# Performance work log

Hardware: AMD Instinct MI355X
Metric: run time of the kernel (lower is better)

Reference implementation:

```python
import jax, jax.numpy as jnp
import numpy as np

NUM_HEADS = 8


def setup_inputs() -> dict:
    key = jax.random.key(0)
    ks = jax.random.split(key, 8)
    B, N, D, H = 4, 1200, 256, NUM_HEADS
    return {
        "query_bbox": jax.random.normal(ks[0], (B, N, 10), jnp.float32) * 20.0,
        "query_feat": jax.random.normal(ks[1], (B, N, D), jnp.float32),
        "beta_w": jax.random.normal(ks[2], (H, D), jnp.float32) * 0.02,
        "beta_b": jax.random.uniform(ks[3], (H,), jnp.float32, 0.0, 2.0),
        "in_proj_w": jax.random.normal(ks[4], (3 * D, D), jnp.float32) * (D ** -0.5),
        "in_proj_b": jnp.zeros((3 * D,), jnp.float32),
        "out_proj_w": jax.random.normal(ks[5], (D, D), jnp.float32) * (D ** -0.5),
        "out_proj_b": jnp.zeros((D,), jnp.float32),
    }


def reference(query_bbox, query_feat, beta_w, beta_b, in_proj_w, in_proj_b,
              out_proj_w, out_proj_b):
    B, N, D = query_feat.shape
    H = NUM_HEADS
    hd = D // H

    # center_dists (no_grad in original): negative pairwise L2 of bbox centers
    centers = jax.lax.stop_gradient(query_bbox[..., :2])            # [B,N,2]
    diff = centers[:, :, None, :] - centers[:, None, :, :]          # [B,N,N,2]
    dist = -jnp.sqrt(jnp.sum(diff * diff, axis=-1))                 # [B,N,N]

    # per-head learned beta scale
    beta = jnp.einsum('bnd,hd->bhn', query_feat, beta_w) + beta_b[None, :, None]  # [B,H,N]
    attn_mask = dist[:, None, :, :] * beta[..., None]               # [B,H,N,N]

    # multi-head self-attention with additive mask
    qkv = jnp.einsum('bnd,ed->bne', query_feat, in_proj_w) + in_proj_b
    q, k, v = jnp.split(qkv, 3, axis=-1)
    q = q.reshape(B, N, H, hd)
    k = k.reshape(B, N, H, hd)
    v = v.reshape(B, N, H, hd)

    scores = jnp.einsum('bqhd,bkhd->bhqk', q, k) * (hd ** -0.5) + attn_mask
    attn = jax.nn.softmax(scores, axis=-1)                          # [B,H,N,N]
    out = jnp.einsum('bhqk,bkhd->bqhd', attn, v).reshape(B, N, D)
    return jnp.einsum('bnd,ed->bne', out, out_proj_w) + out_proj_b
```

## Files before the change

### kernel.cpp

```cpp
#include <hip/hip_runtime.h>
#include <hip/hip_bf16.h>

#define BC 4
#define NQ 1200
#define DIM 256
#define NH 8
#define HD 32
#define E3 768
#define MROWS (BC*NQ)
#define SCALE 0.17677669529663687f
#define L2E 1.4426950408889634f
#define SL2E (SCALE * L2E)

#define VT2_PER_BH 40960
#define VT2_PER_HH 20480

typedef __attribute__((ext_vector_type(8))) short bf16x8;
typedef __attribute__((ext_vector_type(4))) float f32x4;
typedef __attribute__((ext_vector_type(2))) unsigned u32x2;
typedef __attribute__((ext_vector_type(4))) unsigned u32x4;

__device__ inline short f2bf(float f) {
    __hip_bfloat16 h = __float2bfloat16(f);
    return *reinterpret_cast<short*>(&h);
}
__device__ __forceinline__ unsigned cvtpk(float lo, float hi) {
    unsigned r;
    asm("v_cvt_pk_bf16_f32 %0, %1, %2" : "=v"(r) : "v"(lo), "v"(hi));
    return r;
}

__device__ __forceinline__ void gll16(const void* g, void* l) {
    __builtin_amdgcn_global_load_lds(
        (const __attribute__((address_space(1))) unsigned*)g,
        (__attribute__((address_space(3))) unsigned*)l, 16, 0, 0);
}

__global__ void beta_ctr_kernel(const float* __restrict__ feat, const float* __restrict__ bw,
                                const float* __restrict__ bb, const float* __restrict__ bbox,
                                float* __restrict__ beta, float* __restrict__ ctr) {
    int gw = (blockIdx.x * 256 + threadIdx.x) >> 6;
    int lane = threadIdx.x & 63;
    if (gw >= MROWS) return;
    const float* frow = feat + (size_t)gw * DIM;
    float acc[NH];
#pragma unroll
    for (int h = 0; h < NH; ++h) acc[h] = 0.f;
#pragma unroll
    for (int it = 0; it < DIM / 64; ++it) {
        int d = it * 64 + lane;
        float f = frow[d];
#pragma unroll
        for (int h = 0; h < NH; ++h) acc[h] += f * bw[h * DIM + d];
    }
#pragma unroll
    for (int h = 0; h < NH; ++h) {
#pragma unroll
        for (int off = 32; off; off >>= 1) acc[h] += __shfl_xor(acc[h], off);
    }
    int b = gw / NQ, n = gw % NQ;
#pragma unroll
    for (int h = 0; h < NH; ++h) {
        float v = acc[h] + bb[h];
        if (lane == h) beta[(b * NH + h) * NQ + n] = v;
    }
    if (lane == 0) {
        ctr[gw * 2]     = bbox[(size_t)gw * 10];
        ctr[gw * 2 + 1] = bbox[(size_t)gw * 10 + 1];
    }
}

template<bool AF32, bool BF32, bool OUTF32, bool VTOUT, bool QSCALE>
__global__ __launch_bounds__(256) void gemm_k256(const void* __restrict__ Av,
                                                 const void* __restrict__ Bv,
                                                 const float* __restrict__ bias,
                                                 void* __restrict__ Cout, int Edim,
                                                 short* __restrict__ vtout) {
    __shared__ short as[64][40];
    __shared__ short bs[64][40];
    int m0 = blockIdx.y * 64, e0 = blockIdx.x * 64;
    int t = threadIdx.x, lane = t & 63, wid = t >> 6;
    int wr = (wid >> 1) * 32, wc = (wid & 1) * 32;
    f32x4 acc[2][2] = {};
    int lrow = t >> 2, lch = t & 3;
    const float qs = (QSCALE && e0 < DIM) ? SL2E : 1.f;

    for (int ks = 0; ks < DIM / 32; ++ks) {
        bf16x8 av, wv;
        if (AF32) {
            const float* A = (const float*)Av;
            float4 f0 = *(const float4*)(A + (size_t)(m0 + lrow) * DIM + ks * 32 + lch * 8);
            float4 f1 = *(const float4*)(A + (size_t)(m0 + lrow) * DIM + ks * 32 + lch * 8 + 4);
            u32x4 p = {cvtpk(f0.x, f0.y), cvtpk(f0.z, f0.w),
                       cvtpk(f1.x, f1.y), cvtpk(f1.z, f1.w)};
            av = __builtin_bit_cast(bf16x8, p);
        } else {
            av = *(const bf16x8*)((const short*)Av + (size_t)(m0 + lrow) * DIM + ks * 32 + lch * 8);
        }
        if (BF32) {
            const float* B = (const float*)Bv;
            float4 f0 = *(const float4*)(B + (size_t)(e0 + lrow) * DIM + ks * 32 + lch * 8);
            float4 f1 = *(const float4*)(B + (size_t)(e0 + lrow) * DIM + ks * 32 + lch * 8 + 4);
            u32x4 p = {cvtpk(f0.x * qs, f0.y * qs), cvtpk(f0.z * qs, f0.w * qs),
                       cvtpk(f1.x * qs, f1.y * qs), cvtpk(f1.z * qs, f1.w * qs)};
            wv = __builtin_bit_cast(bf16x8, p);
        } else {
            wv = *(const bf16x8*)((const short*)Bv + (size_t)(e0 + lrow) * DIM + ks * 32 + lch * 8);
        }
        __syncthreads();
        *(bf16x8*)&as[lrow][lch * 8] = av;
        *(bf16x8*)&bs[lrow][lch * 8] = wv;
        __syncthreads();
#pragma unroll
        for (int sm = 0; sm < 2; ++sm) {
            bf16x8 af = *(const bf16x8*)&as[wr + sm * 16 + (lane & 15)][(lane >> 4) * 8];
#pragma unroll
            for (int sn = 0; sn < 2; ++sn) {
                bf16x8 bfv = *(const bf16x8*)&bs[wc + sn * 16 + (lane & 15)][(lane >> 4) * 8];
                acc[sm][sn] = __builtin_amdgcn_mfma_f32_16x16x32_bf16(af, bfv, acc[sm][sn], 0, 0, 0);
            }
        }
    }
#pragma unroll
    for (int sm = 0; sm < 2; ++sm)
#pragma unroll
        for (int sn = 0; sn < 2; ++sn) {
            int e = e0 + wc + sn * 16 + (lane & 15);
            float bv = bias[e];
            if (QSCALE && e < DIM) bv *= SL2E;
            float vals[4];
            int mbase = m0 + wr + sm * 16 + (lane >> 4) * 4;
#pragma unroll
            for (int r = 0; r < 4; ++r) vals[r] = acc[sm][sn][r] + bv;
            if (VTOUT && e >= 2 * DIM) {
                int dv = e - 2 * DIM;
                int hv = dv >> 5, dd = dv & 31;
                int hh = dd >> 4, di = dd & 15;
                int bb = mbase / NQ, nn = mbase - bb * NQ;
                u32x2 o = {cvtpk(vals[0], vals[1]), cvtpk(vals[2], vals[3])};
                size_t off = (size_t)(bb * NH + hv) * VT2_PER_BH + hh * VT2_PER_HH
                           + (nn >> 3) * 128 + di * 8 + (nn & 7);
                *(u32x2*)&vtout[off] = o;
            } else {
#pragma unroll
                for (int r = 0; r < 4; ++r) {
                    int m = mbase + r;
                    if (OUTF32) ((float*)Cout)[(size_t)m * Edim + e] = vals[r];
                    else        ((short*)Cout)[(size_t)m * Edim + e] = f2bf(vals[r]);
                }
            }
        }
}

#define BUFSZ 17408
#define KT_OFF 0
#define VT_OFF 8192
#define CK_OFF 16384
#define PL_OFF (2*BUFSZ)
__global__ __launch_bounds__(256, 4) void attn_kernel(const short* __restrict__ qkv,
                                                      const short* __restrict__ vt2,
                                                      const float* __restrict__ beta,
                                                      const float* __restrict__ ctr,
                                                      short* __restrict__ attnb) {
    __shared__ __align__(16) char smem[2 * BUFSZ + 4096];

    const int t = threadIdx.x, lane = t & 63, w = t >> 6;
    const int g = lane >> 4, i = lane & 15;
    const int qg = w >> 1, ksp = w & 1;
    const int bh = blockIdx.y, b = bh >> 3, h = bh & 7;
    const int q0 = blockIdx.x * 32 + qg * 16;
    const int q = q0 + i, qc = min(q, NQ - 1);
    const int kwb = ksp * 64;
    const int bq = b * NQ;

    bf16x8 qf = *(const bf16x8*)(qkv + (size_t)(bq + qc) * E3 + h * HD + g * 8);
    const float cqx = ctr[(bq + qc) * 2];
    const float cqy = ctr[(bq + qc) * 2 + 1];
    const float nbql = -beta[(b * NH + h) * NQ + qc] * L2E;

    const short onebf = (short)0x3F80;
    const bf16x8 ones = {onebf, onebf, onebf, onebf, onebf, onebf, onebf, onebf};

    float mcur = 0.f;
    f32x4 o0 = {}, o1 = {}, oS = {};

    const int koff = ((t >> 6) << 4) + (t & 15);
    const short* kld0 = qkv + (size_t)bq * E3 + DIM + h * HD + (size_t)koff * E3 + ((t >> 4) & 3) * 8;
    const short* kld1 = kld0 + (size_t)64 * E3;
    const short* vld0 = vt2 + (size_t)bh * VT2_PER_BH + (((t >> 4) & 15)) * 128 + (t & 15) * 8;
    const short* vld1 = vld0 + VT2_PER_HH;
    const char*  cld  = (const char*)(ctr + (size_t)bq * 2) + lane * 16;

    auto stage_issue = [&](int base) {
        gll16(kld0, &smem[base + KT_OFF + t * 16]);
        gll16(kld1, &smem[base + KT_OFF + (t + 256) * 16]);
        gll16(vld0, &smem[base + VT_OFF + t * 16]);
        gll16(vld1, &smem[base + VT_OFF + (t + 256) * 16]);
        if (w == 0) gll16(cld, &smem[base + CK_OFF + lane * 16]);
        kld0 += (size_t)128 * E3; kld1 += (size_t)128 * E3;
        vld0 += 2048; vld1 += 2048; cld += 1024;
    };

    stage_issue(0);
    __syncthreads();
    int cur = 0;

    for (int kb = 0; kb < NQ; kb += 128) {
        const bool haveNext = (kb + 128 < NQ);
        const bool tail = (kb + 128 > NQ);
        if (haveNext) stage_issue((cur ^ 1) * BUFSZ);

        const int cb = cur * BUFSZ;
        float st[16];
        f32x4 cinit = {-mcur, -mcur, -mcur, -mcur};
#pragma unroll
        for (int kcl = 0; kcl < 4; ++kcl) {
            bf16x8 af = *(const bf16x8*)&smem[cb + KT_OFF + (((ksp * 4 + kcl) * 64 + lane) << 4)];
            f32x4 s = __builtin_amdgcn_mfma_f32_16x16x32_bf16(af, qf, cinit, 0, 0, 0);
            int lk = kwb + kcl * 16 + 4 * g;
            float4 cA = *(const float4*)&smem[cb + CK_OFF + lk * 8];
            float4 cB = *(const float4*)&smem[cb + CK_OFF + lk * 8 + 16];
            float cxv[4] = {cA.x, cA.z, cB.x, cB.z};
            float cyv[4] = {cA.y, cA.w, cB.y, cB.w};
#pragma unroll
            for (int r = 0; r < 4; ++r) {
                float dx = cqx - cxv[r], dy = cqy - cyv[r];
                float d2 = __builtin_fmaf(dx, dx, dy * dy);
                float dist = __builtin_amdgcn_sqrtf(d2);
                st[kcl * 4 + r] = __builtin_fmaf(dist, nbql, s[r]);
            }
            if (tail) {
#pragma unroll
                for (int r = 0; r < 4; ++r)
                    if (kb + lk + r >= NQ) st[kcl * 4 + r] = -1e30f;
            }
        }

        float a0 = fmaxf(fmaxf(st[0],  st[1]),  st[2]);
        float a1 = fmaxf(fmaxf(st[3],  st[4]),  st[5]);
        float a2 = fmaxf(fmaxf(st[6],  st[7]),  st[8]);
        float a3 = fmaxf(fmaxf(st[9],  st[10]), st[11]);
        float a4 = fmaxf(fmaxf(st[12], st[13]), st[14]);
        float vm = fmaxf(fmaxf(fmaxf(a0, a1), a2), fmaxf(fmaxf(a3, a4), st[15]));
        if (!__all(vm <= 8.0f)) {
            float vr = fmaxf(vm, __shfl_xor(vm, 16));
            vr = fmaxf(vr, __shfl_xor(vr, 32));
            float dm = fmaxf(vr, 0.f);
            float al = __builtin_amdgcn_exp2f(-dm);
            mcur += dm;
#pragma unroll
            for (int r = 0; r < 4; ++r) { o0[r] *= al; o1[r] *= al; }
            oS[0] *= al;
#pragma unroll
            for (int x = 0; x < 16; ++x) st[x] -= dm;
        }
#pragma unroll
        for (int x = 0; x < 16; ++x) st[x] = __builtin_amdgcn_exp2f(st[x]);

#pragma unroll
        for (int kc2 = 0; kc2 < 2; ++kc2) {
#pragma unroll
            for (int kk = 0; kk < 2; ++kk) {
                int kcl = 2 * kc2 + kk;
                u32x2 pw = {cvtpk(st[kcl * 4 + 0], st[kcl * 4 + 1]),
                            cvtpk(st[kcl * 4 + 2], st[kcl * 4 + 3])};
                *(u32x2*)&smem[PL_OFF + (w << 10) + (((kk << 1) + (g >> 1)) << 8) + (i << 4) + ((g & 1) << 3)] = pw;
            }
            bf16x8 pbf = *(const bf16x8*)&smem[PL_OFF + (w << 10) + (g << 8) + (i << 4)];
            int vidx = (8 * ksp + 4 * kc2 + g) * 16 + i;
            bf16x8 vf0 = *(const bf16x8*)&smem[cb + VT_OFF + (vidx << 4)];
            bf16x8 vf1 = *(const bf16x8*)&smem[cb + VT_OFF + ((256 + vidx) << 4)];
            __builtin_amdgcn_s_setprio(1);
            o0 = __builtin_amdgcn_mfma_f32_16x16x32_bf16(vf0, pbf, o0, 0, 0, 0);
            o1 = __builtin_amdgcn_mfma_f32_16x16x32_bf16(vf1, pbf, o1, 0, 0, 0);
            oS = __builtin_amdgcn_mfma_f32_16x16x32_bf16(ones, pbf, oS, 0, 0, 0);
            __builtin_amdgcn_s_setprio(0);
        }

        __syncthreads();
        cur ^= 1;
    }

    float lsum = oS[0];
    float* mrg = (float*)smem;
    float* my = mrg + (w * 64 + lane) * 10;
    my[0] = mcur; my[1] = lsum;
#pragma unroll
    for (int r = 0; r < 4; ++r) { my[2 + r] = o0[r]; my[6 + r] = o1[r]; }
    __syncthreads();
    const float* pr = mrg + ((w ^ 1) * 64 + lane) * 10;
    float m2 = pr[0], l2 = pr[1];
    float mN = fmaxf(mcur, m2);
    float a1 = __builtin_amdgcn_exp2f(mcur - mN);
    float a2 = __builtin_amdgcn_exp2f(m2 - mN);
    float inv = 1.f / (lsum * a1 + l2 * a2);
    int hh = w & 1;
    f32x4 mine = hh ? o1 : o0;
    if (q < NQ) {
        float vals[4];
#pragma unroll
        for (int r = 0; r < 4; ++r) vals[r] = (mine[r] * a1 + pr[2 + hh * 4 + r] * a2) * inv;
        u32x2 outv = {cvtpk(vals[0], vals[1]), cvtpk(vals[2], vals[3])};
        *(u32x2*)&attnb[(size_t)(bq + q) * DIM + h * HD + hh * 16 + 4 * g] = outv;
    }
}

extern "C" void kernel_launch(void* const* d_in, const int* in_sizes, int n_in,
                              void* d_out, int out_size, void* d_ws, size_t ws_size,
                              hipStream_t stream) {
    const float* bbox  = (const float*)d_in[0];
    const float* feat  = (const float*)d_in[1];
    const float* bw    = (const float*)d_in[2];
    const float* bb    = (const float*)d_in[3];
    const float* in_w  = (const float*)d_in[4];
    const float* in_b  = (const float*)d_in[5];
    const float* out_w = (const float*)d_in[6];
    const float* out_b = (const float*)d_in[7];
    float* out = (float*)d_out;

    char* ws = (char*)d_ws;
    size_t off = 0;
    auto alloc = [&](size_t bytes) { void* p = ws + off; off += (bytes + 255) & ~255ull; return p; };
    short* qkvb  = (short*)alloc((size_t)MROWS * E3 * 2);
    short* vtb   = (short*)alloc((size_t)BC * NH * VT2_PER_BH * 2);
    short* attnb = (short*)alloc((size_t)MROWS * DIM * 2);
    float* betab = (float*)alloc((size_t)BC * NH * NQ * 4);
    float* ctr   = (float*)alloc((size_t)BC * NQ * 2 * 4 + 1024);
    (void)ws_size; (void)in_sizes; (void)n_in; (void)out_size;

    beta_ctr_kernel<<<MROWS / 4, 256, 0, stream>>>(feat, bw, bb, bbox, betab, ctr);
    gemm_k256<true, true, false, true, true><<<dim3(E3 / 64, MROWS / 64), 256, 0, stream>>>(feat, in_w, in_b, qkvb, E3, vtb);
    attn_kernel<<<dim3((NQ + 31) / 32, BC * NH), 256, 0, stream>>>(qkvb, vtb, betab, ctr, attnb);
    gemm_k256<false, true, true, false, false><<<dim3(DIM / 64, MROWS / 64), 256, 0, stream>>>(attnb, out_w, out_b, out, DIM, nullptr);
}
```

Baseline: 60.74 us.

## Replace LDS P-transpose with permlane swaps and read centers from global

Replaces the LDS round-trip used to reshape the softmax probabilities into MFMA B-operand layout with permlane32/permlane16 swap instructions, when the compiler provides them. Key-center coordinates are now loaded straight from global memory instead of being staged into LDS by one wave. Together these cut the LDS footprint per block, and launch bounds are raised from 4 to 5 blocks per CU to target higher occupancy. The cost is extra global loads per tile, more register pressure under the tighter launch bound, and reliance on the permlane lane mapping matching the previous LDS layout.

```diff
diff --git a/kernel.cpp b/kernel.cpp
--- a/kernel.cpp
+++ b/kernel.cpp
@@ -19,6 +19,12 @@
 typedef __attribute__((ext_vector_type(4))) float f32x4;
 typedef __attribute__((ext_vector_type(2))) unsigned u32x2;
 typedef __attribute__((ext_vector_type(4))) unsigned u32x4;
+
+#if __has_builtin(__builtin_amdgcn_permlane32_swap) && __has_builtin(__builtin_amdgcn_permlane16_swap)
+#define HAVE_PERMLANE 1
+#else
+#define HAVE_PERMLANE 0
+#endif
 
 __device__ inline short f2bf(float f) {
     __hip_bfloat16 h = __float2bfloat16(f);
@@ -152,17 +158,21 @@
         }
 }
 
-#define BUFSZ 17408
 #define KT_OFF 0
 #define VT_OFF 8192
-#define CK_OFF 16384
+#define BUFSZ 16384
+#if HAVE_PERMLANE
+#define SMEM_SZ (2*BUFSZ)
+#else
 #define PL_OFF (2*BUFSZ)
-__global__ __launch_bounds__(256, 4) void attn_kernel(const short* __restrict__ qkv,
+#define SMEM_SZ (2*BUFSZ + 4096)
+#endif
+__global__ __launch_bounds__(256, 5) void attn_kernel(const short* __restrict__ qkv,
                                                       const short* __restrict__ vt2,
                                                       const float* __restrict__ beta,
                                                       const float* __restrict__ ctr,
                                                       short* __restrict__ attnb) {
-    __shared__ __align__(16) char smem[2 * BUFSZ + 4096];
+    __shared__ __align__(16) char smem[SMEM_SZ];
 
     const int t = threadIdx.x, lane = t & 63, w = t >> 6;
     const int g = lane >> 4, i = lane & 15;
@@ -189,16 +199,15 @@
     const short* kld1 = kld0 + (size_t)64 * E3;
     const short* vld0 = vt2 + (size_t)bh * VT2_PER_BH + (((t >> 4) & 15)) * 128 + (t & 15) * 8;
     const short* vld1 = vld0 + VT2_PER_HH;
-    const char*  cld  = (const char*)(ctr + (size_t)bq * 2) + lane * 16;
+    const float* cgb = ctr + (size_t)bq * 2;
 
     auto stage_issue = [&](int base) {
         gll16(kld0, &smem[base + KT_OFF + t * 16]);
         gll16(kld1, &smem[base + KT_OFF + (t + 256) * 16]);
         gll16(vld0, &smem[base + VT_OFF + t * 16]);
         gll16(vld1, &smem[base + VT_OFF + (t + 256) * 16]);
-        if (w == 0) gll16(cld, &smem[base + CK_OFF + lane * 16]);
         kld0 += (size_t)128 * E3; kld1 += (size_t)128 * E3;
-        vld0 += 2048; vld1 += 2048; cld += 1024;
+        vld0 += 2048; vld1 += 2048;
     };
 
     stage_issue(0);
@@ -217,9 +226,9 @@
         for (int kcl = 0; kcl < 4; ++kcl) {
             bf16x8 af = *(const bf16x8*)&smem[cb + KT_OFF + (((ksp * 4 + kcl) * 64 + lane) << 4)];
             f32x4 s = __builtin_amdgcn_mfma_f32_16x16x32_bf16(af, qf, cinit, 0, 0, 0);
-            int lk = kwb + kcl * 16 + 4 * g;
-            float4 cA = *(const float4*)&smem[cb + CK_OFF + lk * 8];
-            float4 cB = *(const float4*)&smem[cb + CK_OFF + lk * 8 + 16];
+            int kidx = kb + kwb + kcl * 16 + 4 * g;
+            float4 cA = *(const float4*)(cgb + (size_t)kidx * 2);
+            float4 cB = *(const float4*)(cgb + (size_t)kidx * 2 + 4);
             float cxv[4] = {cA.x, cA.z, cB.x, cB.z};
             float cyv[4] = {cA.y, cA.w, cB.y, cB.w};
 #pragma unroll
@@ -232,7 +241,7 @@
             if (tail) {
 #pragma unroll
                 for (int r = 0; r < 4; ++r)
-                    if (kb + lk + r >= NQ) st[kcl * 4 + r] = -1e30f;
+                    if (kidx + r >= NQ) st[kcl * 4 + r] = -1e30f;
             }
         }
 
@@ -257,16 +266,32 @@
 #pragma unroll
         for (int x = 0; x < 16; ++x) st[x] = __builtin_amdgcn_exp2f(st[x]);
 
+        unsigned pk0[4], pk1[4];
+#pragma unroll
+        for (int kcl = 0; kcl < 4; ++kcl) {
+            pk0[kcl] = cvtpk(st[kcl * 4 + 0], st[kcl * 4 + 1]);
+            pk1[kcl] = cvtpk(st[kcl * 4 + 2], st[kcl * 4 + 3]);
+        }
+
 #pragma unroll
         for (int kc2 = 0; kc2 < 2; ++kc2) {
+            bf16x8 pbf;
+#if HAVE_PERMLANE
+            u32x2 aa = __builtin_amdgcn_permlane32_swap(pk0[2 * kc2], pk0[2 * kc2 + 1], false, false);
+            u32x2 bbp = __builtin_amdgcn_permlane16_swap(aa[0], aa[1], false, false);
+            u32x2 cc = __builtin_amdgcn_permlane32_swap(pk1[2 * kc2], pk1[2 * kc2 + 1], false, false);
+            u32x2 ddp = __builtin_amdgcn_permlane16_swap(cc[0], cc[1], false, false);
+            u32x4 pv = {bbp[0], ddp[0], bbp[1], ddp[1]};
+            pbf = __builtin_bit_cast(bf16x8, pv);
+#else
 #pragma unroll
             for (int kk = 0; kk < 2; ++kk) {
                 int kcl = 2 * kc2 + kk;
-                u32x2 pw = {cvtpk(st[kcl * 4 + 0], st[kcl * 4 + 1]),
-                            cvtpk(st[kcl * 4 + 2], st[kcl * 4 + 3])};
+                u32x2 pw = {pk0[kcl], pk1[kcl]};
                 *(u32x2*)&smem[PL_OFF + (w << 10) + (((kk << 1) + (g >> 1)) << 8) + (i << 4) + ((g & 1) << 3)] = pw;
             }
-            bf16x8 pbf = *(const bf16x8*)&smem[PL_OFF + (w << 10) + (g << 8) + (i << 4)];
+            pbf = *(const bf16x8*)&smem[PL_OFF + (w << 10) + (g << 8) + (i << 4)];
+#endif
             int vidx = (8 * ksp + 4 * kc2 + g) * 16 + i;
             bf16x8 vf0 = *(const bf16x8*)&smem[cb + VT_OFF + (vidx << 4)];
             bf16x8 vf1 = *(const bf16x8*)&smem[cb + VT_OFF + ((256 + vidx) << 4)];
```

After: 71.94 us. 18.4% more time.
